# Kernel optimization log

Measured on AMD Instinct MI355X. Metric: run time of the kernel, lower is better.

The kernel has to match this reference:

```python
import jax, jax.numpy as jnp
import numpy as np
from itertools import product

B = 2
X, Y, Z = 96, 96, 192          # voxel grid (x, y, t)
NPB = 300_000                   # occupied voxels per batch item
PX, PY, PZ = X // 2, Y // 2, Z // 4  # pooled grid (kernel/stride [2,2,4])
CIN, COUT, KVOL, NCONV = 32, 64, 27, 2
EPS = 1e-5


def _build_maps():
    """Builds sparse coordinates, maxpool segment ids and 3x3x3 conv kernel maps
    (gather/scatter index pairs per kernel offset), mirroring MinkowskiEngine's
    coordinate manager."""
    rng = np.random.default_rng(0)
    coords = []
    for b in range(B):
        lin = rng.choice(X * Y * Z, NPB, replace=False)
        x = lin // (Y * Z)
        y = (lin // Z) % Y
        z = lin % Z
        coords.append(np.stack([np.full(NPB, b), x, y, z], 1))
    c = np.concatenate(coords).astype(np.int64)  # [N,4] (b,x,y,z)
    # max-pool coord map: out coord = (x//2, y//2, z//4)
    pk = ((c[:, 0] * PX + c[:, 1] // 2) * PY + c[:, 2] // 2) * PZ + c[:, 3] // 4
    uniq, inv = np.unique(pk, return_inverse=True)
    M = len(uniq)
    pz = uniq % PZ
    py = (uniq // PZ) % PY
    px = (uniq // (PZ * PY)) % PX
    pb = uniq // (PZ * PY * PX)
    lut = np.full(B * PX * PY * PZ, -1, np.int64)
    lut[uniq] = np.arange(M)
    ins, outs = [], []
    for dx, dy, dz in product((-1, 0, 1), repeat=3):
        nx, ny, nz = px + dx, py + dy, pz + dz
        ok = (nx >= 0) & (nx < PX) & (ny >= 0) & (ny < PY) & (nz >= 0) & (nz < PZ)
        nk = ((pb * PX + np.clip(nx, 0, PX - 1)) * PY + np.clip(ny, 0, PY - 1)) * PZ + np.clip(nz, 0, PZ - 1)
        j = np.where(ok, lut[nk], -1)
        sel = j >= 0
        ins.append(j[sel])
        outs.append(np.arange(M)[sel])
    L = max(len(a) for a in ins)
    ci = np.full((KVOL, L), M, np.int64)  # pad -> index M (zero row)
    co = np.full((KVOL, L), M, np.int64)  # pad -> dummy out row M (dropped)
    for k in range(KVOL):
        ci[k, : len(ins[k])] = ins[k]
        co[k, : len(outs[k])] = outs[k]
    return inv.astype(np.int64), ci, co, M


def setup_inputs() -> dict:
    key = jax.random.key(0)
    ks = jax.random.split(key, 4)
    pool_seg, ci, co, M = _build_maps()
    N = B * NPB
    feats = jax.random.normal(ks[0], (N, CIN), jnp.float32)
    Wd = jax.random.normal(ks[1], (CIN, COUT), jnp.float32) / np.sqrt(CIN)
    W1 = jax.random.normal(ks[2], (KVOL, COUT, COUT), jnp.float32) / np.sqrt(KVOL * COUT)
    W2 = jax.random.normal(ks[3], (KVOL, COUT, COUT), jnp.float32) / np.sqrt(KVOL * COUT)
    ones = jnp.ones((COUT,), jnp.float32)
    zeros = jnp.zeros((COUT,), jnp.float32)
    return {
        "feats": feats, "Wd": Wd,
        "g0": ones, "b0": zeros,
        "W1": W1, "g1": ones, "b1": zeros,
        "W2": W2, "g2": ones, "b2": zeros,
        "pool_seg": jnp.asarray(pool_seg),
        "conv_in": jnp.asarray(ci), "conv_out": jnp.asarray(co),
        "num_pooled": int(M),
    }


def _bn(h, g, b):
    # training-mode batch norm over all sparse points (biased variance, eps=1e-5)
    m = h.mean(0)
    v = jnp.mean((h - m) ** 2, 0)
    return (h - m) * (g / jnp.sqrt(v + EPS)) + b


def _sparse_conv(h, W, conv_in, conv_out, M):
    # gather-GEMM-scatter over 27 kernel offsets (MinkowskiConvolution, bias=False)
    C = W.shape[-1]
    hp = jnp.concatenate([h, jnp.zeros((1, h.shape[1]), h.dtype)])  # zero pad row
    out = jnp.zeros((M + 1, C), h.dtype)
    for k in range(W.shape[0]):
        out = out.at[conv_out[k]].add(hp[conv_in[k]] @ W[k])
    return out[:M]


def reference(feats, Wd, g0, b0, W1, g1, b1, W2, g2, b2,
              pool_seg, conv_in, conv_out, num_pooled):
    # down_conv (1x1, bias=False) -> BN -> ELU
    h = jax.nn.elu(_bn(feats @ Wd, g0, b0))
    # MinkowskiMaxPooling kernel=stride=[2,2,4] == segment max over pooled cells
    down = jax.ops.segment_max(h, pool_seg, num_segments=num_pooled)
    # nConvs LUConv blocks: ELU(BN(conv3x3x3(x)))
    o = down
    for W, g, b in ((W1, g1, b1), (W2, g2, b2)):
        o = jax.nn.elu(_bn(_sparse_conv(o, W, conv_in, conv_out, num_pooled), g, b))
    # residual add + ELU
    return jax.nn.elu(o + down)
```

## Files before the change

kernel.cpp:

```cpp
#include <hip/hip_runtime.h>
#include <math.h>

#define CIN  32
#define COUT 64
#define KVOL 27
#define EPSF 1e-5f

typedef __attribute__((ext_vector_type(8))) short          short8;
typedef __attribute__((ext_vector_type(8))) unsigned short u16x8;
typedef __attribute__((ext_vector_type(4))) float          float4v;

__device__ __forceinline__ float eluf(float x) { return x > 0.f ? x : expm1f(x); }

__device__ __forceinline__ unsigned short f2bf(float x) {
    unsigned u = __float_as_uint(x);
    unsigned r = (u + 0x7FFFu + ((u >> 16) & 1u)) >> 16;
    return (unsigned short)r;
}
__device__ __forceinline__ unsigned pk2bf(float lo, float hi) {
    return (unsigned)f2bf(lo) | ((unsigned)f2bf(hi) << 16);
}
__device__ __forceinline__ float bf2f(unsigned short h) {
    return __uint_as_float(((unsigned)h) << 16);
}

__global__ void cvt_w_kernel(const float* __restrict__ W1, const float* __restrict__ W2,
                             const float* __restrict__ Wd,
                             unsigned short* __restrict__ Wt1, unsigned short* __restrict__ Wt2,
                             unsigned short* __restrict__ Wdt)
{
    int b = blockIdx.x;
    int t = threadIdx.x;
    if (b == 54) {
        for (int e = t; e < CIN * COUT; e += 256) {
            int i = e >> 6, c = e & 63;
            Wdt[c * CIN + i] = f2bf(Wd[e]);
        }
        return;
    }
    const float* W = (b < 27) ? W1 : W2;
    unsigned short* Wt = (b < 27) ? Wt1 : Wt2;
    int k = (b < 27) ? b : b - 27;
    const float* src = W + (size_t)k * (COUT * COUT);
    unsigned short* dst = Wt + (size_t)k * (COUT * COUT);
    for (int e = t; e < COUT * COUT; e += 256) {
        int i = e >> 6, c = e & 63;
        dst[c * COUT + i] = f2bf(src[e]);
    }
}

__global__ __launch_bounds__(256) void gemm_t_kernel(
    const float* __restrict__ feats, const unsigned short* __restrict__ Wdt,
    int N, unsigned short* __restrict__ t_bf, float* __restrict__ red0)
{
    __shared__ float red_s[64];
    __shared__ float red_q[64];
    int t = threadIdx.x;
    if (t < 64) { red_s[t] = 0.f; red_q[t] = 0.f; }
    __syncthreads();

    int w = t >> 6, lane = t & 63, l15 = lane & 15, quad = lane >> 4;

    short8 aw[4];
    #pragma unroll
    for (int mt = 0; mt < 4; ++mt)
        aw[mt] = *(const short8*)(Wdt + (size_t)(16 * mt + l15) * CIN + quad * 8);

    float s1[16], sq[16];
    #pragma unroll
    for (int e = 0; e < 16; ++e) { s1[e] = 0.f; sq[e] = 0.f; }

    int numTiles = (N + 15) >> 4;
    int stride = gridDim.x * 4;
    int tile = blockIdx.x * 4 + w;

    float4 c0 = make_float4(0.f, 0.f, 0.f, 0.f), c1 = c0;
    {
        int pt = tile * 16 + l15;
        if (tile < numTiles && pt < N) {
            const float4* s = (const float4*)(feats + (size_t)pt * CIN + quad * 8);
            c0 = s[0]; c1 = s[1];
        }
    }

    while (tile < numTiles) {
        int nt = tile + stride;
        float4 n0 = make_float4(0.f, 0.f, 0.f, 0.f), n1 = n0;
        {
            int npt = nt * 16 + l15;
            if (nt < numTiles && npt < N) {
                const float4* s = (const float4*)(feats + (size_t)npt * CIN + quad * 8);
                n0 = s[0]; n1 = s[1];
            }
        }
        union { short8 v; unsigned u[4]; } b;
        b.u[0] = pk2bf(c0.x, c0.y);
        b.u[1] = pk2bf(c0.z, c0.w);
        b.u[2] = pk2bf(c1.x, c1.y);
        b.u[3] = pk2bf(c1.z, c1.w);

        float4v acc[4];
        #pragma unroll
        for (int mt = 0; mt < 4; ++mt)
            acc[mt] = __builtin_amdgcn_mfma_f32_16x16x32_bf16(
                aw[mt], b.v, (float4v){0.f, 0.f, 0.f, 0.f}, 0, 0, 0);

        int pt = tile * 16 + l15;
        if (pt < N) {
            #pragma unroll
            for (int mt = 0; mt < 4; ++mt) {
                uint2 o;
                o.x = pk2bf(acc[mt][0], acc[mt][1]);
                o.y = pk2bf(acc[mt][2], acc[mt][3]);
                *(uint2*)(t_bf + (size_t)pt * COUT + mt * 16 + quad * 4) = o;
            }
        }
        #pragma unroll
        for (int mt = 0; mt < 4; ++mt)
            #pragma unroll
            for (int e = 0; e < 4; ++e) {
                float v = acc[mt][e];
                s1[mt * 4 + e] += v; sq[mt * 4 + e] += v * v;
            }
        c0 = n0; c1 = n1;
        tile = nt;
    }

    #pragma unroll
    for (int m = 1; m <= 8; m <<= 1) {
        #pragma unroll
        for (int e = 0; e < 16; ++e) {
            s1[e] += __shfl_xor(s1[e], m);
            sq[e] += __shfl_xor(sq[e], m);
        }
    }
    if (l15 == 0) {
        #pragma unroll
        for (int e = 0; e < 16; ++e) {
            int ch = (e >> 2) * 16 + quad * 4 + (e & 3);
            atomicAdd(&red_s[ch], s1[e]);
            atomicAdd(&red_q[ch], sq[e]);
        }
    }
    __syncthreads();
    float* dst = red0 + (size_t)(blockIdx.x & 3) * 128;
    if (t < 64)       atomicAdd(&dst[t], red_s[t]);
    else if (t < 128) atomicAdd(&dst[t], red_q[t - 64]);
}

__global__ void fin0_kernel(const float* __restrict__ red, const float* __restrict__ g,
                            const float* __restrict__ b, float* __restrict__ scale,
                            float* __restrict__ shift, int cnt)
{
    int c = threadIdx.x;
    float s = 0.f, q = 0.f;
    #pragma unroll
    for (int i = 0; i < 4; ++i) { s += red[i * 128 + c]; q += red[i * 128 + 64 + c]; }
    float m = s / (float)cnt;
    float var = q / (float)cnt - m * m;
    float sc = g[c] / sqrtf(var + EPSF);
    scale[c] = sc;
    shift[c] = b[c] - m * sc;
}

__global__ void bucket_kernel(const int* __restrict__ pool_seg,
                              int* __restrict__ cnt, int* __restrict__ bucket, int N)
{
    int j = blockIdx.x * 256 + threadIdx.x;
    if (j < N) {
        int s = pool_seg[j];
        int pos = atomicAdd(&cnt[s], 1);
        bucket[(size_t)s * 16 + pos] = j;
    }
}

__global__ __launch_bounds__(256) void pool_max_kernel(
    const unsigned short* __restrict__ t_bf,
    const int* __restrict__ cnt, const int* __restrict__ bucket,
    const float* __restrict__ scale0, const float* __restrict__ shift0,
    unsigned short* __restrict__ down_bf, int M)
{
    int id = blockIdx.x * 256 + threadIdx.x;
    int s = id >> 4, cg = id & 15;
    if (s >= M) return;
    int n = cnt[s];
    const int4* bk4 = (const int4*)(bucket + (size_t)s * 16);
    float4 mx = make_float4(-INFINITY, -INFINITY, -INFINITY, -INFINITY);
    float4 mn = make_float4( INFINITY,  INFINITY,  INFINITY,  INFINITY);
    #pragma unroll
    for (int ch = 0; ch < 4; ++ch) {
        if (ch * 4 >= n) break;
        int4 b4 = bk4[ch];
        #pragma unroll
        for (int e = 0; e < 4; ++e) {
            int p = ch * 4 + e;
            if (p < n) {
                int idx = (e == 0) ? b4.x : (e == 1) ? b4.y : (e == 2) ? b4.z : b4.w;
                ushort4 v = *(const ushort4*)(t_bf + (size_t)idx * COUT + cg * 4);
                float f0 = bf2f(v.x), f1 = bf2f(v.y), f2 = bf2f(v.z), f3 = bf2f(v.w);
                mx.x = fmaxf(mx.x, f0); mn.x = fminf(mn.x, f0);
                mx.y = fmaxf(mx.y, f1); mn.y = fminf(mn.y, f1);
                mx.z = fmaxf(mx.z, f2); mn.z = fminf(mn.z, f2);
                mx.w = fmaxf(mx.w, f3); mn.w = fminf(mn.w, f3);
            }
        }
    }
    int c0 = cg * 4;
    float4 sc = *(const float4*)(scale0 + c0);
    float4 sh = *(const float4*)(shift0 + c0);
    ushort4 o;
    o.x = f2bf(eluf(sc.x * (sc.x >= 0.f ? mx.x : mn.x) + sh.x));
    o.y = f2bf(eluf(sc.y * (sc.y >= 0.f ? mx.y : mn.y) + sh.y));
    o.z = f2bf(eluf(sc.z * (sc.z >= 0.f ? mx.z : mn.z) + sh.z));
    o.w = f2bf(eluf(sc.w * (sc.w >= 0.f ? mx.w : mn.w) + sh.w));
    *(ushort4*)(down_bf + (size_t)s * COUT + c0) = o;
}

__global__ void nbr_kernel(const int* __restrict__ conv_out, const int* __restrict__ conv_in,
                           int* __restrict__ nbrT, int L, int M)
{
    int k = blockIdx.y;
    int idx = blockIdx.x * 256 + threadIdx.x;
    if (idx < L) {
        int e = k * L + idx;
        int j = conv_out[e];
        if (j < M) nbrT[(size_t)k * M + j] = conv_in[e];
    }
}

__global__ void bn_elu_cvt_kernel(const float* __restrict__ o1,
                                  const float* __restrict__ scale,
                                  const float* __restrict__ shift,
                                  unsigned short* __restrict__ o1t, int n4)
{
    int i = blockIdx.x * 256 + threadIdx.x;
    if (i < n4) {
        float4 v = ((const float4*)o1)[i];
        int c0 = (i & 15) * 4;
        float4 sc = *(const float4*)(scale + c0);
        float4 sh = *(const float4*)(shift + c0);
        ushort4 o;
        o.x = f2bf(eluf(v.x * sc.x + sh.x));
        o.y = f2bf(eluf(v.y * sc.y + sh.y));
        o.z = f2bf(eluf(v.z * sc.z + sh.z));
        o.w = f2bf(eluf(v.w * sc.w + sh.w));
        ((ushort4*)o1t)[i] = o;
    }
}

__global__ __launch_bounds__(512) void conv_mfma_kernel(
    const unsigned short* __restrict__ in, const unsigned short* __restrict__ Wt,
    const int* __restrict__ nbrT, int M,
    float* __restrict__ out, float* __restrict__ red)
{
    __shared__ __align__(16) unsigned short A_lds[2][256 * 64];
    __shared__ __align__(16) unsigned short W_lds[2][64 * 64];
    int t = threadIdx.x;

    int nwg = gridDim.x;
    int q = nwg >> 3, r = nwg & 7;
    int xcd = blockIdx.x & 7, pos = blockIdx.x >> 3;
    int sb = (xcd < r ? xcd * (q + 1) : r * (q + 1) + (xcd - r) * q) + pos;
    int base = sb * 256;

    int w = t >> 6, lane = t & 63, l15 = lane & 15, quad = lane >> 4;

    float4v acc[2][4];
    #pragma unroll
    for (int s = 0; s < 2; ++s)
        #pragma unroll
        for (int n = 0; n < 4; ++n)
            acc[s][n] = (float4v){0.f, 0.f, 0.f, 0.f};

    int ar = t >> 1, ah = t & 1;
    int gj = base + ar;
    int arx = ar & 7;
    int wc = t >> 3, wq = t & 7;
    int wcx = wc & 7;

    const u16x8 z8 = (u16x8){0, 0, 0, 0, 0, 0, 0, 0};

    {
        int idx0 = (gj < M) ? nbrT[gj] : -1;
        u16x8 a0 = z8, a1 = z8, a2 = z8, a3 = z8;
        if (idx0 >= 0) {
            const u16x8* src = (const u16x8*)(in + (size_t)idx0 * COUT + 32 * ah);
            a0 = src[0]; a1 = src[1]; a2 = src[2]; a3 = src[3];
        }
        u16x8 w0 = *(const u16x8*)(Wt + (size_t)wc * COUT + wq * 8);

        unsigned short* Ab = A_lds[0];
        *(u16x8*)(Ab + ar * 64 + ((ah * 4 + 0) ^ arx) * 8) = a0;
        *(u16x8*)(Ab + ar * 64 + ((ah * 4 + 1) ^ arx) * 8) = a1;
        *(u16x8*)(Ab + ar * 64 + ((ah * 4 + 2) ^ arx) * 8) = a2;
        *(u16x8*)(Ab + ar * 64 + ((ah * 4 + 3) ^ arx) * 8) = a3;
        *(u16x8*)(W_lds[0] + wc * 64 + ((wq ^ wcx) * 8)) = w0;
    }
    int idxN = (gj < M) ? nbrT[(size_t)M + gj] : -1;
    __syncthreads();

    for (int k = 0; k < KVOL; ++k) {
        int cur = k & 1;
        bool pf = (k + 1 < KVOL);

        u16x8 na0 = z8, na1 = z8, na2 = z8, na3 = z8, nw0 = z8;
        if (pf) {
            if (idxN >= 0) {
                const u16x8* src = (const u16x8*)(in + (size_t)idxN * COUT + 32 * ah);
                na0 = src[0]; na1 = src[1]; na2 = src[2]; na3 = src[3];
            }
            nw0 = *(const u16x8*)(Wt + (size_t)(k + 1) * (COUT * COUT) + (size_t)wc * COUT + wq * 8);
            idxN = (k + 2 < KVOL && gj < M) ? nbrT[(size_t)(k + 2) * M + gj] : -1;
        }

        const unsigned short* Ab = A_lds[cur];
        const unsigned short* Wb = W_lds[cur];
        #pragma unroll
        for (int kk = 0; kk < 64; kk += 32) {
            int slb = quad + (kk >> 3);
            int r0 = 32 * w + l15;
            short8 a0 = *(const short8*)(Ab + r0 * 64 + ((slb ^ (r0 & 7)) * 8));
            int r1 = r0 + 16;
            short8 a1 = *(const short8*)(Ab + r1 * 64 + ((slb ^ (r1 & 7)) * 8));
            #pragma unroll
            for (int n = 0; n < 4; ++n) {
                int rb = 16 * n + l15;
                short8 b = *(const short8*)(Wb + rb * 64 + ((slb ^ (rb & 7)) * 8));
                acc[0][n] = __builtin_amdgcn_mfma_f32_16x16x32_bf16(a0, b, acc[0][n], 0, 0, 0);
                acc[1][n] = __builtin_amdgcn_mfma_f32_16x16x32_bf16(a1, b, acc[1][n], 0, 0, 0);
            }
        }

        if (pf) {
            unsigned short* An = A_lds[cur ^ 1];
            *(u16x8*)(An + ar * 64 + ((ah * 4 + 0) ^ arx) * 8) = na0;
            *(u16x8*)(An + ar * 64 + ((ah * 4 + 1) ^ arx) * 8) = na1;
            *(u16x8*)(An + ar * 64 + ((ah * 4 + 2) ^ arx) * 8) = na2;
            *(u16x8*)(An + ar * 64 + ((ah * 4 + 3) ^ arx) * 8) = na3;
            *(u16x8*)(W_lds[cur ^ 1] + wc * 64 + ((wq ^ wcx) * 8)) = nw0;
        }
        __syncthreads();
    }

    #pragma unroll
    for (int s = 0; s < 2; ++s) {
        int row = base + 32 * w + 16 * s + quad * 4;
        #pragma unroll
        for (int n = 0; n < 4; ++n) {
            int c = 16 * n + l15;
            #pragma unroll
            for (int e = 0; e < 4; ++e)
                if (row + e < M) out[(size_t)(row + e) * COUT + c] = acc[s][n][e];
        }
    }

    float* red_s = (float*)(W_lds[0]);
    float* red_q = red_s + 64;
    if (t < 128) red_s[t] = 0.f;
    __syncthreads();
    #pragma unroll
    for (int n = 0; n < 4; ++n) {
        float s1 = 0.f, sq = 0.f;
        #pragma unroll
        for (int s = 0; s < 2; ++s)
            #pragma unroll
            for (int e = 0; e < 4; ++e) { float v = acc[s][n][e]; s1 += v; sq += v * v; }
        s1 += __shfl_xor(s1, 16); sq += __shfl_xor(sq, 16);
        s1 += __shfl_xor(s1, 32); sq += __shfl_xor(sq, 32);
        if (quad == 0) {
            atomicAdd(&red_s[16 * n + l15], s1);
            atomicAdd(&red_q[16 * n + l15], sq);
        }
    }
    __syncthreads();
    if (t < 64)       atomicAdd(&red[t], red_s[t]);
    else if (t < 128) atomicAdd(&red[t], red_q[t - 64]);
}

__global__ void finC_kernel(const float* __restrict__ red, const float* __restrict__ g,
                            const float* __restrict__ b, float* __restrict__ scale,
                            float* __restrict__ shift, int M)
{
    int c = threadIdx.x;
    float m = red[c] / (float)M;
    float var = red[64 + c] / (float)M - m * m;
    float sc = g[c] / sqrtf(var + EPSF);
    scale[c] = sc;
    shift[c] = b[c] - m * sc;
}

__global__ void final_kernel(float* __restrict__ out, const unsigned short* __restrict__ down_bf,
                             const float* __restrict__ scale2, const float* __restrict__ shift2,
                             int n4)
{
    int i = blockIdx.x * 256 + threadIdx.x;
    if (i < n4) {
        float4 v = ((const float4*)out)[i];
        ushort4 d = ((const ushort4*)down_bf)[i];
        int c0 = (i & 15) * 4;
        float4 sc = *(const float4*)(scale2 + c0);
        float4 sh = *(const float4*)(shift2 + c0);
        v.x = eluf(eluf(v.x * sc.x + sh.x) + bf2f(d.x));
        v.y = eluf(eluf(v.y * sc.y + sh.y) + bf2f(d.y));
        v.z = eluf(eluf(v.z * sc.z + sh.z) + bf2f(d.z));
        v.w = eluf(eluf(v.w * sc.w + sh.w) + bf2f(d.w));
        ((float4*)out)[i] = v;
    }
}

extern "C" void kernel_launch(void* const* d_in, const int* in_sizes, int n_in,
                              void* d_out, int out_size, void* d_ws, size_t ws_size,
                              hipStream_t stream)
{
    (void)n_in; (void)ws_size;
    const float* feats    = (const float*)d_in[0];
    const float* Wd       = (const float*)d_in[1];
    const float* g0       = (const float*)d_in[2];
    const float* b0       = (const float*)d_in[3];
    const float* W1       = (const float*)d_in[4];
    const float* g1       = (const float*)d_in[5];
    const float* b1       = (const float*)d_in[6];
    const float* W2       = (const float*)d_in[7];
    const float* g2       = (const float*)d_in[8];
    const float* b2       = (const float*)d_in[9];
    const int*   pool_seg = (const int*)d_in[10];
    const int*   conv_in  = (const int*)d_in[11];
    const int*   conv_out = (const int*)d_in[12];

    int N = in_sizes[0] / CIN;
    int M = out_size / COUT;
    int L = in_sizes[11] / KVOL;

    char* ws = (char*)d_ws;
    size_t off = 0;
    auto alloc = [&](size_t bytes) -> void* {
        void* p = ws + off;
        off = (off + bytes + 255) & ~(size_t)255;
        return p;
    };
    float*          o1      = (float*)alloc((size_t)M * COUT * 4);
    unsigned short* down_bf = (unsigned short*)alloc((size_t)M * COUT * 2);
    unsigned short* o1t     = (unsigned short*)alloc((size_t)M * COUT * 2);
    unsigned short* t_bf    = (unsigned short*)alloc((size_t)N * COUT * 2);
    int*            nbrT    = (int*)alloc((size_t)KVOL * M * 4);
    unsigned short* Wt1     = (unsigned short*)alloc((size_t)KVOL * COUT * COUT * 2);
    unsigned short* Wt2     = (unsigned short*)alloc((size_t)KVOL * COUT * COUT * 2);
    unsigned short* Wdt     = (unsigned short*)alloc((size_t)CIN * COUT * 2);
    int*            cnt     = (int*)alloc((size_t)M * 4);
    int*            bucket  = (int*)alloc((size_t)M * 16 * 4);
    float* red  = (float*)alloc((size_t)768 * 4);
    float* red0 = red, *red1 = red + 512, *red2 = red + 640;
    float* sreg = (float*)alloc((size_t)6 * 64 * 4);
    float* scale0 = sreg, *shift0 = sreg + 64;
    float* scale1 = sreg + 128, *shift1 = sreg + 192;
    float* scale2 = sreg + 256, *shift2 = sreg + 320;

    hipMemsetAsync(nbrT, 0xFF, (size_t)KVOL * M * 4, stream);
    hipMemsetAsync(cnt, 0, (size_t)M * 4, stream);
    hipMemsetAsync(red, 0, (size_t)768 * 4, stream);

    cvt_w_kernel<<<55, 256, 0, stream>>>(W1, W2, Wd, Wt1, Wt2, Wdt);
    gemm_t_kernel<<<1024, 256, 0, stream>>>(feats, Wdt, N, t_bf, red0);
    fin0_kernel<<<1, 64, 0, stream>>>(red0, g0, b0, scale0, shift0, N);
    bucket_kernel<<<(N + 255) / 256, 256, 0, stream>>>(pool_seg, cnt, bucket, N);
    pool_max_kernel<<<(M * 16 + 255) / 256, 256, 0, stream>>>(
        t_bf, cnt, bucket, scale0, shift0, down_bf, M);
    dim3 gn((L + 255) / 256, KVOL);
    nbr_kernel<<<gn, 256, 0, stream>>>(conv_out, conv_in, nbrT, L, M);

    int cblocks = (M + 255) / 256;
    conv_mfma_kernel<<<cblocks, 512, 0, stream>>>(down_bf, Wt1, nbrT, M, o1, red1);
    finC_kernel<<<1, 64, 0, stream>>>(red1, g1, b1, scale1, shift1, M);
    int n4 = (M * COUT) / 4;
    bn_elu_cvt_kernel<<<(n4 + 255) / 256, 256, 0, stream>>>(o1, scale1, shift1, o1t, n4);
    conv_mfma_kernel<<<cblocks, 512, 0, stream>>>(o1t, Wt2, nbrT, M, (float*)d_out, red2);
    finC_kernel<<<1, 64, 0, stream>>>(red2, g2, b2, scale2, shift2, M);
    final_kernel<<<(n4 + 255) / 256, 256, 0, stream>>>(
        (float*)d_out, down_bf, scale2, shift2, n4);
}
```

Before: 491.3 us.

## Fuse prep kernels, fold BN finalize into consumers, deepen conv gather prefetch

Merges weight conversion, pool bucketing and neighbour-map building into one prep launch. The three BN-finalize micro-kernels are removed and each consumer computes scale and shift into shared memory. The two memsets are merged into one by placing cnt and red next to each other. The conv kernel now prefetches neighbour indices further ahead and keeps gathered rows in registers two steps in advance, to hide gather latency. This removes about five launches and their gaps, at the cost of redundant per-block BN math and more register pressure in the conv kernel.

```diff
diff --git a/kernel.cpp b/kernel.cpp
--- a/kernel.cpp
+++ b/kernel.cpp
@@ -24,28 +24,52 @@
     return __uint_as_float(((unsigned)h) << 16);
 }
 
-__global__ void cvt_w_kernel(const float* __restrict__ W1, const float* __restrict__ W2,
-                             const float* __restrict__ Wd,
-                             unsigned short* __restrict__ Wt1, unsigned short* __restrict__ Wt2,
-                             unsigned short* __restrict__ Wdt)
-{
-    int b = blockIdx.x;
-    int t = threadIdx.x;
-    if (b == 54) {
-        for (int e = t; e < CIN * COUT; e += 256) {
+__global__ void prep_kernel(const float* __restrict__ W1, const float* __restrict__ W2,
+                            const float* __restrict__ Wd,
+                            unsigned short* __restrict__ Wt1, unsigned short* __restrict__ Wt2,
+                            unsigned short* __restrict__ Wdt,
+                            const int* __restrict__ pool_seg, int* __restrict__ cnt,
+                            int* __restrict__ bucket, int N,
+                            const int* __restrict__ conv_out, const int* __restrict__ conv_in,
+                            int* __restrict__ nbrT, int L, int M, int nbB, int nbL)
+{
+    int b = blockIdx.x, t = threadIdx.x;
+    if (b < 55) {
+        if (b == 54) {
+            for (int e = t; e < CIN * COUT; e += 256) {
+                int i = e >> 6, c = e & 63;
+                Wdt[c * CIN + i] = f2bf(Wd[e]);
+            }
+            return;
+        }
+        const float* W = (b < 27) ? W1 : W2;
+        unsigned short* Wt = (b < 27) ? Wt1 : Wt2;
+        int k = (b < 27) ? b : b - 27;
+        const float* src = W + (size_t)k * (COUT * COUT);
+        unsigned short* dst = Wt + (size_t)k * (COUT * COUT);
+        for (int e = t; e < COUT * COUT; e += 256) {
             int i = e >> 6, c = e & 63;
-            Wdt[c * CIN + i] = f2bf(Wd[e]);
+            dst[c * COUT + i] = f2bf(src[e]);
         }
         return;
     }
-    const float* W = (b < 27) ? W1 : W2;
-    unsigned short* Wt = (b < 27) ? Wt1 : Wt2;
-    int k = (b < 27) ? b : b - 27;
-    const float* src = W + (size_t)k * (COUT * COUT);
-    unsigned short* dst = Wt + (size_t)k * (COUT * COUT);
-    for (int e = t; e < COUT * COUT; e += 256) {
-        int i = e >> 6, c = e & 63;
-        dst[c * COUT + i] = f2bf(src[e]);
+    b -= 55;
+    if (b < nbB) {
+        int j = b * 256 + t;
+        if (j < N) {
+            int s = pool_seg[j];
+            int pos = atomicAdd(&cnt[s], 1);
+            bucket[(size_t)s * 16 + pos] = j;
+        }
+        return;
+    }
+    b -= nbB;
+    int k = b / nbL, blk = b - k * nbL;
+    int idx = blk * 256 + t;
+    if (idx < L) {
+        int e = k * L + idx;
+        int j = conv_out[e];
+        if (j < M) nbrT[(size_t)k * M + j] = conv_in[e];
     }
 }
 
@@ -148,39 +172,28 @@
     else if (t < 128) atomicAdd(&dst[t], red_q[t - 64]);
 }
 
-__global__ void fin0_kernel(const float* __restrict__ red, const float* __restrict__ g,
-                            const float* __restrict__ b, float* __restrict__ scale,
-                            float* __restrict__ shift, int cnt)
-{
-    int c = threadIdx.x;
-    float s = 0.f, q = 0.f;
-    #pragma unroll
-    for (int i = 0; i < 4; ++i) { s += red[i * 128 + c]; q += red[i * 128 + 64 + c]; }
-    float m = s / (float)cnt;
-    float var = q / (float)cnt - m * m;
-    float sc = g[c] / sqrtf(var + EPSF);
-    scale[c] = sc;
-    shift[c] = b[c] - m * sc;
-}
-
-__global__ void bucket_kernel(const int* __restrict__ pool_seg,
-                              int* __restrict__ cnt, int* __restrict__ bucket, int N)
-{
-    int j = blockIdx.x * 256 + threadIdx.x;
-    if (j < N) {
-        int s = pool_seg[j];
-        int pos = atomicAdd(&cnt[s], 1);
-        bucket[(size_t)s * 16 + pos] = j;
-    }
-}
-
 __global__ __launch_bounds__(256) void pool_max_kernel(
     const unsigned short* __restrict__ t_bf,
     const int* __restrict__ cnt, const int* __restrict__ bucket,
-    const float* __restrict__ scale0, const float* __restrict__ shift0,
-    unsigned short* __restrict__ down_bf, int M)
-{
-    int id = blockIdx.x * 256 + threadIdx.x;
+    const float* __restrict__ red0, const float* __restrict__ g0,
+    const float* __restrict__ b0,
+    unsigned short* __restrict__ down_bf, int M, int N)
+{
+    __shared__ float sc_s[64], sh_s[64];
+    int t = threadIdx.x;
+    if (t < 64) {
+        float s = 0.f, q2 = 0.f;
+        #pragma unroll
+        for (int i = 0; i < 4; ++i) { s += red0[i * 128 + t]; q2 += red0[i * 128 + 64 + t]; }
+        float m = s / (float)N;
+        float var = q2 / (float)N - m * m;
+        float sc = g0[t] / sqrtf(var + EPSF);
+        sc_s[t] = sc;
+        sh_s[t] = b0[t] - m * sc;
+    }
+    __syncthreads();
+
+    int id = blockIdx.x * 256 + t;
     int s = id >> 4, cg = id & 15;
     if (s >= M) return;
     int n = cnt[s];
@@ -206,45 +219,69 @@
         }
     }
     int c0 = cg * 4;
-    float4 sc = *(const float4*)(scale0 + c0);
-    float4 sh = *(const float4*)(shift0 + c0);
+    float scx = sc_s[c0], scy = sc_s[c0 + 1], scz = sc_s[c0 + 2], scw = sc_s[c0 + 3];
+    float shx = sh_s[c0], shy = sh_s[c0 + 1], shz = sh_s[c0 + 2], shw = sh_s[c0 + 3];
     ushort4 o;
-    o.x = f2bf(eluf(sc.x * (sc.x >= 0.f ? mx.x : mn.x) + sh.x));
-    o.y = f2bf(eluf(sc.y * (sc.y >= 0.f ? mx.y : mn.y) + sh.y));
-    o.z = f2bf(eluf(sc.z * (sc.z >= 0.f ? mx.z : mn.z) + sh.z));
-    o.w = f2bf(eluf(sc.w * (sc.w >= 0.f ? mx.w : mn.w) + sh.w));
+    o.x = f2bf(eluf(scx * (scx >= 0.f ? mx.x : mn.x) + shx));
+    o.y = f2bf(eluf(scy * (scy >= 0.f ? mx.y : mn.y) + shy));
+    o.z = f2bf(eluf(scz * (scz >= 0.f ? mx.z : mn.z) + shz));
+    o.w = f2bf(eluf(scw * (scw >= 0.f ? mx.w : mn.w) + shw));
     *(ushort4*)(down_bf + (size_t)s * COUT + c0) = o;
 }
 
-__global__ void nbr_kernel(const int* __restrict__ conv_out, const int* __restrict__ conv_in,
-                           int* __restrict__ nbrT, int L, int M)
-{
-    int k = blockIdx.y;
-    int idx = blockIdx.x * 256 + threadIdx.x;
-    if (idx < L) {
-        int e = k * L + idx;
-        int j = conv_out[e];
-        if (j < M) nbrT[(size_t)k * M + j] = conv_in[e];
-    }
-}
-
-__global__ void bn_elu_cvt_kernel(const float* __restrict__ o1,
-                                  const float* __restrict__ scale,
-                                  const float* __restrict__ shift,
-                                  unsigned short* __restrict__ o1t, int n4)
-{
-    int i = blockIdx.x * 256 + threadIdx.x;
+__global__ __launch_bounds__(256) void bn_elu_cvt_kernel(
+    const float* __restrict__ o1, const float* __restrict__ red,
+    const float* __restrict__ g, const float* __restrict__ bb,
+    unsigned short* __restrict__ o1t, int n4, int M)
+{
+    __shared__ float sc_s[64], sh_s[64];
+    int t = threadIdx.x;
+    if (t < 64) {
+        float m = red[t] / (float)M;
+        float var = red[64 + t] / (float)M - m * m;
+        float sc = g[t] / sqrtf(var + EPSF);
+        sc_s[t] = sc;
+        sh_s[t] = bb[t] - m * sc;
+    }
+    __syncthreads();
+    int i = blockIdx.x * 256 + t;
     if (i < n4) {
         float4 v = ((const float4*)o1)[i];
         int c0 = (i & 15) * 4;
-        float4 sc = *(const float4*)(scale + c0);
-        float4 sh = *(const float4*)(shift + c0);
         ushort4 o;
-        o.x = f2bf(eluf(v.x * sc.x + sh.x));
-        o.y = f2bf(eluf(v.y * sc.y + sh.y));
-        o.z = f2bf(eluf(v.z * sc.z + sh.z));
-        o.w = f2bf(eluf(v.w * sc.w + sh.w));
+        o.x = f2bf(eluf(v.x * sc_s[c0]     + sh_s[c0]));
+        o.y = f2bf(eluf(v.y * sc_s[c0 + 1] + sh_s[c0 + 1]));
+        o.z = f2bf(eluf(v.z * sc_s[c0 + 2] + sh_s[c0 + 2]));
+        o.w = f2bf(eluf(v.w * sc_s[c0 + 3] + sh_s[c0 + 3]));
         ((ushort4*)o1t)[i] = o;
+    }
+}
+
+__global__ __launch_bounds__(256) void final_kernel(
+    float* __restrict__ out, const unsigned short* __restrict__ down_bf,
+    const float* __restrict__ red, const float* __restrict__ g,
+    const float* __restrict__ bb, int n4, int M)
+{
+    __shared__ float sc_s[64], sh_s[64];
+    int t = threadIdx.x;
+    if (t < 64) {
+        float m = red[t] / (float)M;
+        float var = red[64 + t] / (float)M - m * m;
+        float sc = g[t] / sqrtf(var + EPSF);
+        sc_s[t] = sc;
+        sh_s[t] = bb[t] - m * sc;
+    }
+    __syncthreads();
+    int i = blockIdx.x * 256 + t;
+    if (i < n4) {
+        float4 v = ((const float4*)out)[i];
+        ushort4 d = ((const ushort4*)down_bf)[i];
+        int c0 = (i & 15) * 4;
+        v.x = eluf(eluf(v.x * sc_s[c0]     + sh_s[c0])     + bf2f(d.x));
+        v.y = eluf(eluf(v.y * sc_s[c0 + 1] + sh_s[c0 + 1]) + bf2f(d.y));
+        v.z = eluf(eluf(v.z * sc_s[c0 + 2] + sh_s[c0 + 2]) + bf2f(d.z));
+        v.w = eluf(eluf(v.w * sc_s[c0 + 3] + sh_s[c0 + 3]) + bf2f(d.w));
+        ((float4*)out)[i] = v;
     }
 }
 
@@ -274,47 +311,63 @@
 
     int ar = t >> 1, ah = t & 1;
     int gj = base + ar;
+    bool gv = (gj < M);
     int arx = ar & 7;
     int wc = t >> 3, wq = t & 7;
     int wcx = wc & 7;
 
+    int awo0 = ar * 64 + (((ah * 4 + 0) ^ arx) * 8);
+    int awo1 = ar * 64 + (((ah * 4 + 1) ^ arx) * 8);
+    int awo2 = ar * 64 + (((ah * 4 + 2) ^ arx) * 8);
+    int awo3 = ar * 64 + (((ah * 4 + 3) ^ arx) * 8);
+    int wwo  = wc * 64 + ((wq ^ wcx) * 8);
+
     const u16x8 z8 = (u16x8){0, 0, 0, 0, 0, 0, 0, 0};
 
-    {
-        int idx0 = (gj < M) ? nbrT[gj] : -1;
-        u16x8 a0 = z8, a1 = z8, a2 = z8, a3 = z8;
-        if (idx0 >= 0) {
-            const u16x8* src = (const u16x8*)(in + (size_t)idx0 * COUT + 32 * ah);
-            a0 = src[0]; a1 = src[1]; a2 = src[2]; a3 = src[3];
-        }
-        u16x8 w0 = *(const u16x8*)(Wt + (size_t)wc * COUT + wq * 8);
-
-        unsigned short* Ab = A_lds[0];
-        *(u16x8*)(Ab + ar * 64 + ((ah * 4 + 0) ^ arx) * 8) = a0;
-        *(u16x8*)(Ab + ar * 64 + ((ah * 4 + 1) ^ arx) * 8) = a1;
-        *(u16x8*)(Ab + ar * 64 + ((ah * 4 + 2) ^ arx) * 8) = a2;
-        *(u16x8*)(Ab + ar * 64 + ((ah * 4 + 3) ^ arx) * 8) = a3;
-        *(u16x8*)(W_lds[0] + wc * 64 + ((wq ^ wcx) * 8)) = w0;
-    }
-    int idxN = (gj < M) ? nbrT[(size_t)M + gj] : -1;
-    __syncthreads();
-
-    for (int k = 0; k < KVOL; ++k) {
-        int cur = k & 1;
-        bool pf = (k + 1 < KVOL);
-
-        u16x8 na0 = z8, na1 = z8, na2 = z8, na3 = z8, nw0 = z8;
-        if (pf) {
-            if (idxN >= 0) {
-                const u16x8* src = (const u16x8*)(in + (size_t)idxN * COUT + 32 * ah);
-                na0 = src[0]; na1 = src[1]; na2 = src[2]; na3 = src[3];
-            }
-            nw0 = *(const u16x8*)(Wt + (size_t)(k + 1) * (COUT * COUT) + (size_t)wc * COUT + wq * 8);
-            idxN = (k + 2 < KVOL && gj < M) ? nbrT[(size_t)(k + 2) * M + gj] : -1;
-        }
-
-        const unsigned short* Ab = A_lds[cur];
-        const unsigned short* Wb = W_lds[cur];
+    int i0 = gv ? nbrT[gj] : -1;
+    int i1 = gv ? nbrT[(size_t)M + gj] : -1;
+    int i2 = gv ? nbrT[(size_t)2 * M + gj] : -1;
+    int i3 = gv ? nbrT[(size_t)3 * M + gj] : -1;
+
+    u16x8 pa0 = z8, pa1 = z8, pa2 = z8, pa3 = z8;
+    if (i0 >= 0) {
+        const u16x8* s = (const u16x8*)(in + (size_t)i0 * COUT + 32 * ah);
+        pa0 = s[0]; pa1 = s[1]; pa2 = s[2]; pa3 = s[3];
+    }
+    u16x8 pw = *(const u16x8*)(Wt + wc * COUT + wq * 8);
+
+    u16x8 ca0 = z8, ca1 = z8, ca2 = z8, ca3 = z8;
+    if (i1 >= 0) {
+        const u16x8* s = (const u16x8*)(in + (size_t)i1 * COUT + 32 * ah);
+        ca0 = s[0]; ca1 = s[1]; ca2 = s[2]; ca3 = s[3];
+    }
+    u16x8 cw = *(const u16x8*)(Wt + (COUT * COUT) + wc * COUT + wq * 8);
+
+    *(u16x8*)(A_lds[0] + awo0) = pa0;
+    *(u16x8*)(A_lds[0] + awo1) = pa1;
+    *(u16x8*)(A_lds[0] + awo2) = pa2;
+    *(u16x8*)(A_lds[0] + awo3) = pa3;
+    *(u16x8*)(W_lds[0] + wwo) = pw;
+    __syncthreads();
+
+    u16x8 na0 = z8, na1 = z8, na2 = z8, na3 = z8, nw = z8;
+
+    auto step = [&](int k,
+                    u16x8& c0, u16x8& c1, u16x8& c2, u16x8& c3, u16x8& cwv,
+                    u16x8& x0, u16x8& x1, u16x8& x2, u16x8& x3, u16x8& xw) {
+        if (k + 2 < KVOL) {
+            x0 = z8; x1 = z8; x2 = z8; x3 = z8;
+            if (i2 >= 0) {
+                const u16x8* s = (const u16x8*)(in + (size_t)i2 * COUT + 32 * ah);
+                x0 = s[0]; x1 = s[1]; x2 = s[2]; x3 = s[3];
+            }
+            xw = *(const u16x8*)(Wt + (size_t)(k + 2) * (COUT * COUT) + wc * COUT + wq * 8);
+        }
+        i2 = i3;
+        i3 = (k + 4 < KVOL && gv) ? nbrT[(size_t)(k + 4) * M + gj] : -1;
+
+        const unsigned short* Ab = A_lds[k & 1];
+        const unsigned short* Wb = W_lds[k & 1];
         #pragma unroll
         for (int kk = 0; kk < 64; kk += 32) {
             int slb = quad + (kk >> 3);
@@ -323,23 +376,29 @@
             int r1 = r0 + 16;
             short8 a1 = *(const short8*)(Ab + r1 * 64 + ((slb ^ (r1 & 7)) * 8));
             #pragma unroll
-            for (int n = 0; n < 4; ++n) {
-                int rb = 16 * n + l15;
-                short8 b = *(const short8*)(Wb + rb * 64 + ((slb ^ (rb & 7)) * 8));
-                acc[0][n] = __builtin_amdgcn_mfma_f32_16x16x32_bf16(a0, b, acc[0][n], 0, 0, 0);
-                acc[1][n] = __builtin_amdgcn_mfma_f32_16x16x32_bf16(a1, b, acc[1][n], 0, 0, 0);
-            }
-        }
-
-        if (pf) {
-            unsigned short* An = A_lds[cur ^ 1];
-            *(u16x8*)(An + ar * 64 + ((ah * 4 + 0) ^ arx) * 8) = na0;
-            *(u16x8*)(An + ar * 64 + ((ah * 4 + 1) ^ arx) * 8) = na1;
-            *(u16x8*)(An + ar * 64 + ((ah * 4 + 2) ^ arx) * 8) = na2;
-            *(u16x8*)(An + ar * 64 + ((ah * 4 + 3) ^ arx) * 8) = na3;
-            *(u16x8*)(W_lds[cur ^ 1] + wc * 64 + ((wq ^ wcx) * 8)) = nw0;
+            for (int nn = 0; nn < 4; ++nn) {
+                int rb = 16 * nn + l15;
+                short8 bfr = *(const short8*)(Wb + rb * 64 + ((slb ^ (rb & 7)) * 8));
+                acc[0][nn] = __builtin_amdgcn_mfma_f32_16x16x32_bf16(a0, bfr, acc[0][nn], 0, 0, 0);
+                acc[1][nn] = __builtin_amdgcn_mfma_f32_16x16x32_bf16(a1, bfr, acc[1][nn], 0, 0, 0);
+            }
+        }
+
+        if (k + 1 < KVOL) {
+            unsigned short* An = A_lds[(k + 1) & 1];
+            *(u16x8*)(An + awo0) = c0;
+            *(u16x8*)(An + awo1) = c1;
+            *(u16x8*)(An + awo2) = c2;
+            *(u16x8*)(An + awo3) = c3;
+            *(u16x8*)(W_lds[(k + 1) & 1] + wwo) = cwv;
         }
         __syncthreads();
+    };
+
+    for (int k = 0; k < KVOL; k += 2) {
+        step(k,     ca0, ca1, ca2, ca3, cw, na0, na1, na2, na3, nw);
+        if (k + 1 < KVOL)
+            step(k + 1, na0, na1, na2, na3, nw, ca0, ca1, ca2, ca3, cw);
     }
 
     #pragma unroll
@@ -375,37 +434,6 @@
     __syncthreads();
     if (t < 64)       atomicAdd(&red[t], red_s[t]);
     else if (t < 128) atomicAdd(&red[t], red_q[t - 64]);
-}
-
-__global__ void finC_kernel(const float* __restrict__ red, const float* __restrict__ g,
-                            const float* __restrict__ b, float* __restrict__ scale,
-                            float* __restrict__ shift, int M)
-{
-    int c = threadIdx.x;
-    float m = red[c] / (float)M;
-    float var = red[64 + c] / (float)M - m * m;
-    float sc = g[c] / sqrtf(var + EPSF);
-    scale[c] = sc;
-    shift[c] = b[c] - m * sc;
-}
-
-__global__ void final_kernel(float* __restrict__ out, const unsigned short* __restrict__ down_bf,
-                             const float* __restrict__ scale2, const float* __restrict__ shift2,
-                             int n4)
-{
-    int i = blockIdx.x * 256 + threadIdx.x;
-    if (i < n4) {
-        float4 v = ((const float4*)out)[i];
-        ushort4 d = ((const ushort4*)down_bf)[i];
-        int c0 = (i & 15) * 4;
-        float4 sc = *(const float4*)(scale2 + c0);
-        float4 sh = *(const float4*)(shift2 + c0);
-        v.x = eluf(eluf(v.x * sc.x + sh.x) + bf2f(d.x));
-        v.y = eluf(eluf(v.y * sc.y + sh.y) + bf2f(d.y));
-        v.z = eluf(eluf(v.z * sc.z + sh.z) + bf2f(d.z));
-        v.w = eluf(eluf(v.w * sc.w + sh.w) + bf2f(d.w));
-        ((float4*)out)[i] = v;
-    }
 }
 
 extern "C" void kernel_launch(void* const* d_in, const int* in_sizes, int n_in,
@@ -446,35 +474,27 @@
     unsigned short* Wt1     = (unsigned short*)alloc((size_t)KVOL * COUT * COUT * 2);
     unsigned short* Wt2     = (unsigned short*)alloc((size_t)KVOL * COUT * COUT * 2);
     unsigned short* Wdt     = (unsigned short*)alloc((size_t)CIN * COUT * 2);
+    int*            bucket  = (int*)alloc((size_t)M * 16 * 4);
     int*            cnt     = (int*)alloc((size_t)M * 4);
-    int*            bucket  = (int*)alloc((size_t)M * 16 * 4);
-    float* red  = (float*)alloc((size_t)768 * 4);
+    float*          red     = (float*)alloc((size_t)768 * 4);
     float* red0 = red, *red1 = red + 512, *red2 = red + 640;
-    float* sreg = (float*)alloc((size_t)6 * 64 * 4);
-    float* scale0 = sreg, *shift0 = sreg + 64;
-    float* scale1 = sreg + 128, *shift1 = sreg + 192;
-    float* scale2 = sreg + 256, *shift2 = sreg + 320;
 
     hipMemsetAsync(nbrT, 0xFF, (size_t)KVOL * M * 4, stream);
-    hipMemsetAsync(cnt, 0, (size_t)M * 4, stream);
-    hipMemsetAsync(red, 0, (size_t)768 * 4, stream);
-
-    cvt_w_kernel<<<55, 256, 0, stream>>>(W1, W2, Wd, Wt1, Wt2, Wdt);
+    hipMemsetAsync(cnt, 0, (size_t)((char*)(red + 768) - (char*)cnt), stream);
+
+    int nbB = (N + 255) / 256, nbL = (L + 255) / 256;
+    prep_kernel<<<55 + nbB + nbL * KVOL, 256, 0, stream>>>(
+        W1, W2, Wd, Wt1, Wt2, Wdt, pool_seg, cnt, bucket, N,
+        conv_out, conv_in, nbrT, L, M, nbB, nbL);
     gemm_t_kernel<<<1024, 256, 0, stream>>>(feats, Wdt, N, t_bf, red0);
-    fin0_kernel<<<1, 64, 0, stream>>>(red0, g0, b0, scale0, shift0, N);
-    bucket_kernel<<<(N + 255) / 256, 256, 0, stream>>>(pool_seg, cnt, bucket, N);
     pool_max_kernel<<<(M * 16 + 255) / 256, 256, 0, stream>>>(
-        t_bf, cnt, bucket, scale0, shift0, down_bf, M);
-    dim3 gn((L + 255) / 256, KVOL);
-    nbr_kernel<<<gn, 256, 0, stream>>>(conv_out, conv_in, nbrT, L, M);
+        t_bf, cnt, bucket, red0, g0, b0, down_bf, M, N);
 
     int cblocks = (M + 255) / 256;
+    int n4 = (M * COUT) / 4;
     conv_mfma_kernel<<<cblocks, 512, 0, stream>>>(down_bf, Wt1, nbrT, M, o1, red1);
-    finC_kernel<<<1, 64, 0, stream>>>(red1, g1, b1, scale1, shift1, M);
-    int n4 = (M * COUT) / 4;
-    bn_elu_cvt_kernel<<<(n4 + 255) / 256, 256, 0, stream>>>(o1, scale1, shift1, o1t, n4);
+    bn_elu_cvt_kernel<<<(n4 + 255) / 256, 256, 0, stream>>>(o1, red1, g1, b1, o1t, n4, M);
     conv_mfma_kernel<<<cblocks, 512, 0, stream>>>(o1t, Wt2, nbrT, M, (float*)d_out, red2);
-    finC_kernel<<<1, 64, 0, stream>>>(red2, g2, b2, scale2, shift2, M);
     final_kernel<<<(n4 + 255) / 256, 256, 0, stream>>>(
-        (float*)d_out, down_bf, scale2, shift2, n4);
-}
+        (float*)d_out, down_bf, red2, g2, b2, n4, M);
+}
```

New measurement: 568.8 us. 15.8% more time.
